# Kernel tuning notes

Measured on AMD Instinct MI355X. Metric: run time of the kernel, lower is better.

The kernel has to match this reference:

```python
import jax, jax.numpy as jnp
import numpy as np

N_NODES = 50000
N_EDGES = 800000
D_FEAT = 96
HIDDEN = 96
N_CLASSES = 2


def setup_inputs() -> dict:
    key = jax.random.key(0)
    k1, k2, k3, k4 = jax.random.split(key, 4)
    x = jax.random.normal(k1, (N_NODES, D_FEAT), dtype=jnp.float32)
    edge_index = jax.random.randint(k2, (2, N_EDGES), 0, N_NODES, dtype=jnp.int64)
    # Linear weights stored as [in, out] (equivalent to torch's W.T)
    W1 = jax.random.normal(k3, (D_FEAT, HIDDEN), dtype=jnp.float32) * (1.0 / np.sqrt(D_FEAT))
    b1 = jnp.zeros((HIDDEN,), dtype=jnp.float32)
    W2 = jax.random.normal(k4, (HIDDEN, N_CLASSES), dtype=jnp.float32) * (1.0 / np.sqrt(HIDDEN))
    b2 = jnp.zeros((N_CLASSES,), dtype=jnp.float32)
    return {"x": x, "edge_index": edge_index, "W1": W1, "b1": b1, "W2": W2, "b2": b2}


def _gin_conv(x, src, dst, W, b, num_nodes):
    # GIN aggregation (eps=0): h_i = (1+eps)*x_i + sum_{j in N(i)} x_j, then Linear
    aggr = jax.ops.segment_sum(x[src], dst, num_segments=num_nodes)  # [N, F]
    h = x + aggr
    return h @ W + b


def reference(x, edge_index, W1, b1, W2, b2):
    src, dst = edge_index[0], edge_index[1]
    n = x.shape[0]
    h = jax.nn.relu(_gin_conv(x, src, dst, W1, b1, n))
    # F.dropout with training=False (eval mode) is identity
    out = _gin_conv(h, src, dst, W2, b2, n)
    return out
```

## Files before the change

kernel.cpp:

```cpp
#include <hip/hip_runtime.h>

#define D 96
#define D4 24
#define NT 64
#define XPAD 97
#define NXCD 8
#define CAP 64

typedef unsigned int uint32;
typedef unsigned short ushort16;
typedef int int4v __attribute__((ext_vector_type(4)));

__device__ __forceinline__ uint32 pk_bf16(float a, float b) {
    uint32 ua = __float_as_uint(a);
    uint32 ub = __float_as_uint(b);
    ua = (ua + 0x7fffu + ((ua >> 16) & 1u)) >> 16;
    ub = (ub + 0x7fffu + ((ub >> 16) & 1u)) & 0xffff0000u;
    return (ua & 0xffffu) | ub;
}

#define UNPK_ADD(u, o) \
    acc[(o)+0] += __uint_as_float((u).x << 16); \
    acc[(o)+1] += __uint_as_float((u).x & 0xffff0000u); \
    acc[(o)+2] += __uint_as_float((u).y << 16); \
    acc[(o)+3] += __uint_as_float((u).y & 0xffff0000u); \
    acc[(o)+4] += __uint_as_float((u).z << 16); \
    acc[(o)+5] += __uint_as_float((u).z & 0xffff0000u); \
    acc[(o)+6] += __uint_as_float((u).w << 16); \
    acc[(o)+7] += __uint_as_float((u).w & 0xffff0000u);

#define UNPK_SET(u, o) \
    acc[(o)+0] = __uint_as_float((u).x << 16); \
    acc[(o)+1] = __uint_as_float((u).x & 0xffff0000u); \
    acc[(o)+2] = __uint_as_float((u).y << 16); \
    acc[(o)+3] = __uint_as_float((u).y & 0xffff0000u); \
    acc[(o)+4] = __uint_as_float((u).z << 16); \
    acc[(o)+5] = __uint_as_float((u).z & 0xffff0000u); \
    acc[(o)+6] = __uint_as_float((u).w << 16); \
    acc[(o)+7] = __uint_as_float((u).w & 0xffff0000u);

__global__ __launch_bounds__(256, 2)
void gemm1_kernel(const float* __restrict__ x,
                  const float* __restrict__ W,
                  ushort16* __restrict__ yq,
                  int* __restrict__ cursor,
                  float2* __restrict__ z, int n) {
    __shared__ float Xs[NT][XPAD];
    __shared__ float4 Ws[D * D4];

    const int tid = threadIdx.x;

    const int t = blockIdx.x * 256 + tid;
    if (t < n) {
        cursor[t] = 0;
        z[t] = make_float2(0.f, 0.f);
    }

    for (int i = tid; i < D * D4; i += 256)
        Ws[i] = ((const float4*)W)[i];

    const int node_l = tid >> 2;
    const int qq = tid & 3;
    const int node = blockIdx.x * NT + node_l;

    if (node < n) {
        const float4* xr = ((const float4*)(x + (size_t)node * D)) + qq * 6;
#pragma unroll
        for (int j = 0; j < 6; ++j) {
            const float4 v = xr[j];
            Xs[node_l][qq * 24 + j * 4 + 0] = v.x;
            Xs[node_l][qq * 24 + j * 4 + 1] = v.y;
            Xs[node_l][qq * 24 + j * 4 + 2] = v.z;
            Xs[node_l][qq * 24 + j * 4 + 3] = v.w;
        }
    }
    __syncthreads();

    if (node < n) {
        float4 oacc[6];
#pragma unroll
        for (int j = 0; j < 6; ++j) oacc[j] = make_float4(0.f, 0.f, 0.f, 0.f);
#pragma unroll 4
        for (int k = 0; k < D; ++k) {
            const float xv = Xs[node_l][k];
            const float4* wrow = Ws + k * D4 + qq * 6;
#pragma unroll
            for (int j = 0; j < 6; ++j) {
                const float4 w = wrow[j];
                oacc[j].x += xv * w.x; oacc[j].y += xv * w.y;
                oacc[j].z += xv * w.z; oacc[j].w += xv * w.w;
            }
        }
        uint32 p[12];
#pragma unroll
        for (int j = 0; j < 6; ++j) {
            p[2 * j + 0] = pk_bf16(oacc[j].x, oacc[j].y);
            p[2 * j + 1] = pk_bf16(oacc[j].z, oacc[j].w);
        }
        uint4* dstp = (uint4*)(yq + ((size_t)qq * n + node) * 24);
        dstp[0] = make_uint4(p[0], p[1], p[2], p[3]);
        dstp[1] = make_uint4(p[4], p[5], p[6], p[7]);
        dstp[2] = make_uint4(p[8], p[9], p[10], p[11]);
    }
}

__global__ __launch_bounds__(256)
void fill_x_kernel(const int* __restrict__ src, const int* __restrict__ dst,
                   int* __restrict__ cursor, int* __restrict__ srcs,
                   int E, int nper, int nGroups) {
    const int xcd = blockIdx.x & (NXCD - 1);
    const int g = blockIdx.x >> 3;
    const int lo = xcd * nper, hi = lo + nper;
    const int4v* dst4 = (const int4v*)dst;
    const int4v* src4 = (const int4v*)src;
    const int quadE = E >> 2;
    for (int i = g * 256 + (int)threadIdx.x; i < quadE; i += nGroups * 256) {
        const int4v dv = __builtin_nontemporal_load(dst4 + i);
        const int4v sv = __builtin_nontemporal_load(src4 + i);
        if (dv.x >= lo && dv.x < hi) {
            const int p = atomicAdd(&cursor[dv.x], 1);
            if (p < CAP) srcs[dv.x * CAP + p] = sv.x;
        }
        if (dv.y >= lo && dv.y < hi) {
            const int p = atomicAdd(&cursor[dv.y], 1);
            if (p < CAP) srcs[dv.y * CAP + p] = sv.y;
        }
        if (dv.z >= lo && dv.z < hi) {
            const int p = atomicAdd(&cursor[dv.z], 1);
            if (p < CAP) srcs[dv.z * CAP + p] = sv.z;
        }
        if (dv.w >= lo && dv.w < hi) {
            const int p = atomicAdd(&cursor[dv.w], 1);
            if (p < CAP) srcs[dv.w * CAP + p] = sv.w;
        }
    }
    if (g == 0 && threadIdx.x == 0) {
        for (int e = E & ~3; e < E; ++e) {
            const int d = dst[e];
            if (d >= lo && d < hi) {
                const int p = atomicAdd(&cursor[d], 1);
                if (p < CAP) srcs[d * CAP + p] = src[e];
            }
        }
    }
}

__global__ __launch_bounds__(256)
void gather1z_kernel(const ushort16* __restrict__ yq,
                     const float* __restrict__ b1,
                     const float* __restrict__ W2,
                     const int* __restrict__ cursor,
                     const int* __restrict__ srcs,
                     float* __restrict__ z,
                     int n, int bpq) {
    const int blk = blockIdx.x;
    const int q = (blk & 7) >> 1;
    const int i = ((blk >> 3) << 1) | (blk & 1);
    if (i >= bpq) return;
    const int tid = threadIdx.x;
    const int node = i * 64 + (tid >> 2);
    const int h = tid & 3;
    if (node >= n) return;

    const uint4* Y = (const uint4*)(yq + (size_t)q * n * 24);

    float acc[24];
    if (h == 0) {
        const uint4* r = Y + (size_t)node * 3;
        const uint4 u0 = r[0], u1 = r[1], u2 = r[2];
        UNPK_SET(u0, 0) UNPK_SET(u1, 8) UNPK_SET(u2, 16)
    } else {
#pragma unroll
        for (int j = 0; j < 24; ++j) acc[j] = 0.f;
    }

    const int s0 = node * CAP;
    const int deg = min(cursor[node], CAP);
    int p = h;
    for (; p + 12 < deg; p += 16) {
        const int sA = srcs[s0 + p];
        const int sB = srcs[s0 + p + 4];
        const int sC = srcs[s0 + p + 8];
        const int sD = srcs[s0 + p + 12];
        const uint4* rA = Y + (size_t)sA * 3;
        const uint4* rB = Y + (size_t)sB * 3;
        const uint4* rC = Y + (size_t)sC * 3;
        const uint4* rD = Y + (size_t)sD * 3;
        const uint4 a0 = rA[0], a1 = rA[1], a2 = rA[2];
        const uint4 c0 = rB[0], c1 = rB[1], c2 = rB[2];
        const uint4 e0 = rC[0], e1 = rC[1], e2 = rC[2];
        const uint4 f0 = rD[0], f1 = rD[1], f2 = rD[2];
        UNPK_ADD(a0, 0) UNPK_ADD(a1, 8) UNPK_ADD(a2, 16)
        UNPK_ADD(c0, 0) UNPK_ADD(c1, 8) UNPK_ADD(c2, 16)
        UNPK_ADD(e0, 0) UNPK_ADD(e1, 8) UNPK_ADD(e2, 16)
        UNPK_ADD(f0, 0) UNPK_ADD(f1, 8) UNPK_ADD(f2, 16)
    }
    for (; p + 4 < deg; p += 8) {
        const int sA = srcs[s0 + p];
        const int sB = srcs[s0 + p + 4];
        const uint4* rA = Y + (size_t)sA * 3;
        const uint4* rB = Y + (size_t)sB * 3;
        const uint4 a0 = rA[0], a1 = rA[1], a2 = rA[2];
        const uint4 c0 = rB[0], c1 = rB[1], c2 = rB[2];
        UNPK_ADD(a0, 0) UNPK_ADD(a1, 8) UNPK_ADD(a2, 16)
        UNPK_ADD(c0, 0) UNPK_ADD(c1, 8) UNPK_ADD(c2, 16)
    }
    if (p < deg) {
        const uint4* rA = Y + (size_t)srcs[s0 + p] * 3;
        const uint4 a0 = rA[0], a1 = rA[1], a2 = rA[2];
        UNPK_ADD(a0, 0) UNPK_ADD(a1, 8) UNPK_ADD(a2, 16)
    }

#pragma unroll
    for (int j = 0; j < 24; ++j) {
        acc[j] += __shfl_xor(acc[j], 1, 64);
        acc[j] += __shfl_xor(acc[j], 2, 64);
    }

    if (h == 0) {
        const float* bq = b1 + q * 24;
        const float* wq = W2 + q * 48;
        float z0 = 0.f, z1 = 0.f;
#pragma unroll
        for (int j = 0; j < 24; ++j) {
            const float hv = fmaxf(acc[j] + bq[j], 0.0f);
            z0 += hv * wq[2 * j + 0];
            z1 += hv * wq[2 * j + 1];
        }
        atomicAdd(&z[2 * node + 0], z0);
        atomicAdd(&z[2 * node + 1], z1);
    }
}

__global__ __launch_bounds__(256)
void gather2_kernel(const float* __restrict__ z,
                    const float* __restrict__ b,
                    const int* __restrict__ cursor,
                    const int* __restrict__ srcs,
                    float* __restrict__ out, int n) {
    const int node = blockIdx.x * blockDim.x + threadIdx.x;
    if (node >= n) return;

    const float2 zi = ((const float2*)z)[node];
    float a0 = zi.x + b[0];
    float a1 = zi.y + b[1];

    const int s0 = node * CAP;
    const int deg = min(cursor[node], CAP);
    int p = 0;
    for (; p + 2 <= deg; p += 2) {
        const float2 vA = ((const float2*)z)[srcs[s0 + p]];
        const float2 vB = ((const float2*)z)[srcs[s0 + p + 1]];
        a0 += vA.x + vB.x;
        a1 += vA.y + vB.y;
    }
    if (p < deg) {
        const float2 vA = ((const float2*)z)[srcs[s0 + p]];
        a0 += vA.x;
        a1 += vA.y;
    }
    ((float2*)out)[node] = make_float2(a0, a1);
}

extern "C" void kernel_launch(void* const* d_in, const int* in_sizes, int n_in,
                              void* d_out, int out_size, void* d_ws, size_t ws_size,
                              hipStream_t stream) {
    const float* x   = (const float*)d_in[0];
    const int*   eix = (const int*)d_in[1];
    const float* W1  = (const float*)d_in[2];
    const float* b1  = (const float*)d_in[3];
    const float* W2  = (const float*)d_in[4];
    const float* b2  = (const float*)d_in[5];
    float*       out = (float*)d_out;

    const int n = in_sizes[0] / D;
    const int E = in_sizes[1] / 2;
    const int* src = eix;
    const int* dst = eix + E;

    const int nper = (n + NXCD - 1) / NXCD;

    ushort16* yq = (ushort16*)d_ws;
    float* z     = (float*)(yq + (size_t)n * D);
    int* cursor  = (int*)(z + 2 * (size_t)n);
    int* srcs    = cursor + n;

    const int nGroups = 1024;

    const int tiles = (n + NT - 1) / NT;
    gemm1_kernel<<<tiles, 256, 0, stream>>>(x, W1, yq, cursor, (float2*)z, n);

    fill_x_kernel<<<nGroups * NXCD, 256, 0, stream>>>(src, dst, cursor, srcs, E, nper, nGroups);

    const int bpq = (n + 63) / 64;
    const int g1grid = 8 * ((bpq + 1) / 2);
    gather1z_kernel<<<g1grid, 256, 0, stream>>>(yq, b1, W2, cursor, srcs, z, n, bpq);

    gather2_kernel<<<(n + 255) / 256, 256, 0, stream>>>(z, b2, cursor, srcs, out, n);
}
```

Before: 117.7 us.

## Fuse GEMM and edge-bucketing into one launch and pad per-node cursors

The first GEMM and the edge bucket-fill kernel are merged into one grid. The first blocks run the GEMM and the remaining blocks do the atomic scatter of source indices, so the two independent phases can run at the same time. Per-node cursors are spread to a 16-int stride so each atomic counter sits on its own cache line, which is meant to cut contention between neighbouring counters. The fill grid shrinks from 1024 to 384 groups per XCD, and a separate init kernel now zeroes the larger cursor array and z. In exchange there is one extra launch, more memory to zero, and strided cursor reads in the gather kernels.

```diff
diff --git a/kernel.cpp b/kernel.cpp
--- a/kernel.cpp
+++ b/kernel.cpp
@@ -6,6 +6,7 @@
 #define XPAD 97
 #define NXCD 8
 #define CAP 64
+#define CSTRIDE 16
 
 typedef unsigned int uint32;
 typedef unsigned short ushort16;
@@ -39,107 +40,110 @@
     acc[(o)+6] = __uint_as_float((u).w << 16); \
     acc[(o)+7] = __uint_as_float((u).w & 0xffff0000u);
 
+__global__ void init_kernel(int4* __restrict__ cur4, float2* __restrict__ z, int n) {
+    const int i = blockIdx.x * blockDim.x + threadIdx.x;
+    const int total4 = n * CSTRIDE / 4;
+    for (int j = i; j < total4; j += gridDim.x * blockDim.x)
+        cur4[j] = make_int4(0, 0, 0, 0);
+    if (i < n) z[i] = make_float2(0.f, 0.f);
+}
+
 __global__ __launch_bounds__(256, 2)
-void gemm1_kernel(const float* __restrict__ x,
+void fused_kernel(const float* __restrict__ x,
                   const float* __restrict__ W,
                   ushort16* __restrict__ yq,
+                  const int* __restrict__ src,
+                  const int* __restrict__ dst,
                   int* __restrict__ cursor,
-                  float2* __restrict__ z, int n) {
+                  int* __restrict__ srcs,
+                  int n, int E, int nper, int gemmBlocks, int nGroups) {
     __shared__ float Xs[NT][XPAD];
     __shared__ float4 Ws[D * D4];
 
+    const int blk = blockIdx.x;
     const int tid = threadIdx.x;
 
-    const int t = blockIdx.x * 256 + tid;
-    if (t < n) {
-        cursor[t] = 0;
-        z[t] = make_float2(0.f, 0.f);
-    }
-
-    for (int i = tid; i < D * D4; i += 256)
-        Ws[i] = ((const float4*)W)[i];
-
-    const int node_l = tid >> 2;
-    const int qq = tid & 3;
-    const int node = blockIdx.x * NT + node_l;
-
-    if (node < n) {
-        const float4* xr = ((const float4*)(x + (size_t)node * D)) + qq * 6;
-#pragma unroll
-        for (int j = 0; j < 6; ++j) {
-            const float4 v = xr[j];
-            Xs[node_l][qq * 24 + j * 4 + 0] = v.x;
-            Xs[node_l][qq * 24 + j * 4 + 1] = v.y;
-            Xs[node_l][qq * 24 + j * 4 + 2] = v.z;
-            Xs[node_l][qq * 24 + j * 4 + 3] = v.w;
-        }
-    }
-    __syncthreads();
-
-    if (node < n) {
-        float4 oacc[6];
-#pragma unroll
-        for (int j = 0; j < 6; ++j) oacc[j] = make_float4(0.f, 0.f, 0.f, 0.f);
+    if (blk < gemmBlocks) {
+        for (int i = tid; i < D * D4; i += 256)
+            Ws[i] = ((const float4*)W)[i];
+
+        const int node_l = tid >> 2;
+        const int qq = tid & 3;
+        const int node = blk * NT + node_l;
+
+        if (node < n) {
+            const float4* xr = ((const float4*)(x + (size_t)node * D)) + qq * 6;
+#pragma unroll
+            for (int j = 0; j < 6; ++j) {
+                const float4 v = xr[j];
+                Xs[node_l][qq * 24 + j * 4 + 0] = v.x;
+                Xs[node_l][qq * 24 + j * 4 + 1] = v.y;
+                Xs[node_l][qq * 24 + j * 4 + 2] = v.z;
+                Xs[node_l][qq * 24 + j * 4 + 3] = v.w;
+            }
+        }
+        __syncthreads();
+
+        if (node < n) {
+            float4 oacc[6];
+#pragma unroll
+            for (int j = 0; j < 6; ++j) oacc[j] = make_float4(0.f, 0.f, 0.f, 0.f);
 #pragma unroll 4
-        for (int k = 0; k < D; ++k) {
-            const float xv = Xs[node_l][k];
-            const float4* wrow = Ws + k * D4 + qq * 6;
+            for (int k = 0; k < D; ++k) {
+                const float xv = Xs[node_l][k];
+                const float4* wrow = Ws + k * D4 + qq * 6;
+#pragma unroll
+                for (int j = 0; j < 6; ++j) {
+                    const float4 w = wrow[j];
+                    oacc[j].x += xv * w.x; oacc[j].y += xv * w.y;
+                    oacc[j].z += xv * w.z; oacc[j].w += xv * w.w;
+                }
+            }
+            uint32 p[12];
 #pragma unroll
             for (int j = 0; j < 6; ++j) {
-                const float4 w = wrow[j];
-                oacc[j].x += xv * w.x; oacc[j].y += xv * w.y;
-                oacc[j].z += xv * w.z; oacc[j].w += xv * w.w;
-            }
-        }
-        uint32 p[12];
-#pragma unroll
-        for (int j = 0; j < 6; ++j) {
-            p[2 * j + 0] = pk_bf16(oacc[j].x, oacc[j].y);
-            p[2 * j + 1] = pk_bf16(oacc[j].z, oacc[j].w);
-        }
-        uint4* dstp = (uint4*)(yq + ((size_t)qq * n + node) * 24);
-        dstp[0] = make_uint4(p[0], p[1], p[2], p[3]);
-        dstp[1] = make_uint4(p[4], p[5], p[6], p[7]);
-        dstp[2] = make_uint4(p[8], p[9], p[10], p[11]);
-    }
-}
-
-__global__ __launch_bounds__(256)
-void fill_x_kernel(const int* __restrict__ src, const int* __restrict__ dst,
-                   int* __restrict__ cursor, int* __restrict__ srcs,
-                   int E, int nper, int nGroups) {
-    const int xcd = blockIdx.x & (NXCD - 1);
-    const int g = blockIdx.x >> 3;
-    const int lo = xcd * nper, hi = lo + nper;
-    const int4v* dst4 = (const int4v*)dst;
-    const int4v* src4 = (const int4v*)src;
-    const int quadE = E >> 2;
-    for (int i = g * 256 + (int)threadIdx.x; i < quadE; i += nGroups * 256) {
-        const int4v dv = __builtin_nontemporal_load(dst4 + i);
-        const int4v sv = __builtin_nontemporal_load(src4 + i);
-        if (dv.x >= lo && dv.x < hi) {
-            const int p = atomicAdd(&cursor[dv.x], 1);
-            if (p < CAP) srcs[dv.x * CAP + p] = sv.x;
-        }
-        if (dv.y >= lo && dv.y < hi) {
-            const int p = atomicAdd(&cursor[dv.y], 1);
-            if (p < CAP) srcs[dv.y * CAP + p] = sv.y;
-        }
-        if (dv.z >= lo && dv.z < hi) {
-            const int p = atomicAdd(&cursor[dv.z], 1);
-            if (p < CAP) srcs[dv.z * CAP + p] = sv.z;
-        }
-        if (dv.w >= lo && dv.w < hi) {
-            const int p = atomicAdd(&cursor[dv.w], 1);
-            if (p < CAP) srcs[dv.w * CAP + p] = sv.w;
-        }
-    }
-    if (g == 0 && threadIdx.x == 0) {
-        for (int e = E & ~3; e < E; ++e) {
-            const int d = dst[e];
-            if (d >= lo && d < hi) {
-                const int p = atomicAdd(&cursor[d], 1);
-                if (p < CAP) srcs[d * CAP + p] = src[e];
+                p[2 * j + 0] = pk_bf16(oacc[j].x, oacc[j].y);
+                p[2 * j + 1] = pk_bf16(oacc[j].z, oacc[j].w);
+            }
+            uint4* dstp = (uint4*)(yq + ((size_t)qq * n + node) * 24);
+            dstp[0] = make_uint4(p[0], p[1], p[2], p[3]);
+            dstp[1] = make_uint4(p[4], p[5], p[6], p[7]);
+            dstp[2] = make_uint4(p[8], p[9], p[10], p[11]);
+        }
+    } else {
+        const int xcd = blk & (NXCD - 1);
+        const int g = (blk - gemmBlocks) >> 3;
+        const int lo = xcd * nper, hi = lo + nper;
+        const int4v* dst4 = (const int4v*)dst;
+        const int4v* src4 = (const int4v*)src;
+        const int quadE = E >> 2;
+        for (int i = g * 256 + tid; i < quadE; i += nGroups * 256) {
+            const int4v dv = __builtin_nontemporal_load(dst4 + i);
+            const int4v sv = __builtin_nontemporal_load(src4 + i);
+            if (dv.x >= lo && dv.x < hi) {
+                const int p = atomicAdd(&cursor[dv.x * CSTRIDE], 1);
+                if (p < CAP) srcs[dv.x * CAP + p] = sv.x;
+            }
+            if (dv.y >= lo && dv.y < hi) {
+                const int p = atomicAdd(&cursor[dv.y * CSTRIDE], 1);
+                if (p < CAP) srcs[dv.y * CAP + p] = sv.y;
+            }
+            if (dv.z >= lo && dv.z < hi) {
+                const int p = atomicAdd(&cursor[dv.z * CSTRIDE], 1);
+                if (p < CAP) srcs[dv.z * CAP + p] = sv.z;
+            }
+            if (dv.w >= lo && dv.w < hi) {
+                const int p = atomicAdd(&cursor[dv.w * CSTRIDE], 1);
+                if (p < CAP) srcs[dv.w * CAP + p] = sv.w;
+            }
+        }
+        if (g == 0 && tid == 0) {
+            for (int e = E & ~3; e < E; ++e) {
+                const int d = dst[e];
+                if (d >= lo && d < hi) {
+                    const int p = atomicAdd(&cursor[d * CSTRIDE], 1);
+                    if (p < CAP) srcs[d * CAP + p] = src[e];
+                }
             }
         }
     }
@@ -175,7 +179,7 @@
     }
 
     const int s0 = node * CAP;
-    const int deg = min(cursor[node], CAP);
+    const int deg = min(cursor[node * CSTRIDE], CAP);
     int p = h;
     for (; p + 12 < deg; p += 16) {
         const int sA = srcs[s0 + p];
@@ -246,7 +250,7 @@
     float a1 = zi.y + b[1];
 
     const int s0 = node * CAP;
-    const int deg = min(cursor[node], CAP);
+    const int deg = min(cursor[node * CSTRIDE], CAP);
     int p = 0;
     for (; p + 2 <= deg; p += 2) {
         const float2 vA = ((const float2*)z)[srcs[s0 + p]];
@@ -283,14 +287,16 @@
     ushort16* yq = (ushort16*)d_ws;
     float* z     = (float*)(yq + (size_t)n * D);
     int* cursor  = (int*)(z + 2 * (size_t)n);
-    int* srcs    = cursor + n;
-
-    const int nGroups = 1024;
-
-    const int tiles = (n + NT - 1) / NT;
-    gemm1_kernel<<<tiles, 256, 0, stream>>>(x, W1, yq, cursor, (float2*)z, n);
-
-    fill_x_kernel<<<nGroups * NXCD, 256, 0, stream>>>(src, dst, cursor, srcs, E, nper, nGroups);
+    int* srcs    = cursor + (size_t)n * CSTRIDE;
+
+    const int gemmBlocks = (n + NT - 1) / NT;
+    const int nGroups = 384;
+    const int fillBlocks = nGroups * NXCD;
+
+    init_kernel<<<784, 256, 0, stream>>>((int4*)cursor, (float2*)z, n);
+
+    fused_kernel<<<gemmBlocks + fillBlocks, 256, 0, stream>>>(
+        x, W1, yq, src, dst, cursor, srcs, n, E, nper, gemmBlocks, nGroups);
 
     const int bpq = (n + 63) / 64;
     const int g1grid = 8 * ((bpq + 1) / 2);
```

Result: slower. 127.2 us (+8.1%).
